# Kernel tuning notes

Measured on AMD Instinct MI355X. Metric: run time of the kernel, lower is better.

Reference implementation:

```python
import jax, jax.numpy as jnp
import numpy as np
import math

D_MODEL = 768
NUM_HEADS = 12
SPARSITY = 0.7


def setup_inputs() -> dict:
    key = jax.random.key(0)
    ks = jax.random.split(key, 9)
    B, S, D = 2, 2048, D_MODEL
    scale = 1.0 / math.sqrt(D)  # xavier-ish
    inp = {
        "x": jax.random.normal(ks[0], (B, S, D), dtype=jnp.float32),
        "Wq": jax.random.normal(ks[1], (D, D), dtype=jnp.float32) * scale,
        "bq": jnp.zeros((D,), dtype=jnp.float32),
        "Wk": jax.random.normal(ks[2], (D, D), dtype=jnp.float32) * scale,
        "bk": jnp.zeros((D,), dtype=jnp.float32),
        "Wv": jax.random.normal(ks[3], (D, D), dtype=jnp.float32) * scale,
        "bv": jnp.zeros((D,), dtype=jnp.float32),
        "Wo": jax.random.normal(ks[4], (D, D), dtype=jnp.float32) * scale,
        "bo": jnp.zeros((D,), dtype=jnp.float32),
    }
    return inp


def reference(x, Wq, bq, Wk, bk, Wv, bv, Wo, bo):
    B, S, D = x.shape
    H = NUM_HEADS
    hd = D // H
    k_keep = max(1, int((1.0 - SPARSITY) * S))

    # projections (nn.Linear: x @ W.T + b), split into heads -> [B,H,S,hd]
    q = (x @ Wq.T + bq).reshape(B, S, H, hd).transpose(0, 2, 1, 3)
    k = (x @ Wk.T + bk).reshape(B, S, H, hd).transpose(0, 2, 1, 3)
    v = (x @ Wv.T + bv).reshape(B, S, H, hd).transpose(0, 2, 1, 3)

    # dense scores [B,H,S,S]
    scores = jnp.einsum("bhqd,bhkd->bhqk", q, k) / math.sqrt(hd)

    # per-row top-k sparsification (training path of the torch module)
    _, topk_idx = jax.lax.top_k(scores, k_keep)  # [B,H,S,k]
    bi = jnp.arange(B)[:, None, None, None]
    hi = jnp.arange(H)[None, :, None, None]
    si = jnp.arange(S)[None, None, :, None]
    keep = jnp.zeros(scores.shape, dtype=bool).at[bi, hi, si, topk_idx].set(True)
    scores = jnp.where(keep, scores, jnp.float32(-1e9))

    attn = jax.nn.softmax(scores, axis=-1)
    out = jnp.einsum("bhqk,bhkd->bhqd", attn, v)  # [B,H,S,hd]
    out = out.transpose(0, 2, 1, 3).reshape(B, S, D)
    return out @ Wo.T + bo
```

## Files before the change

### kernel.cpp

```cpp
#include <hip/hip_runtime.h>
#include <math.h>

#define B_ 2
#define S_ 2048
#define D_ 768
#define H_ 12
#define HD_ 64
#define KKEEP 614
#define M_ (B_*S_)
#define KD_ 768
#define SRW 2072

typedef __attribute__((ext_vector_type(8))) short bf8;
typedef __attribute__((ext_vector_type(4))) float f4;

__device__ __forceinline__ unsigned short f2bf(float f) {
    unsigned u = __float_as_uint(f);
    u += 0x7FFF + ((u >> 16) & 1);
    return (unsigned short)(u >> 16);
}
__device__ __forceinline__ float bf2f(unsigned short h) {
    return __uint_as_float((unsigned)h << 16);
}
__device__ __forceinline__ unsigned pk_sext15(unsigned o) {
    return ((o >> 15) & 0x00010001u) * 0xFFFFu;
}

__global__ void split_kernel(const float* __restrict__ src,
                             unsigned short* __restrict__ hi,
                             unsigned short* __restrict__ lo, int n) {
    int i = blockIdx.x * blockDim.x + threadIdx.x;
    if (i >= n) return;
    float f = src[i];
    unsigned short h = f2bf(f);
    hi[i] = h;
    lo[i] = f2bf(f - bf2f(h));
}

__global__ void split_w_kernel(const float* __restrict__ w0, const float* __restrict__ w1,
                               const float* __restrict__ w2, const float* __restrict__ w3,
                               unsigned short* __restrict__ hi,
                               unsigned short* __restrict__ lo) {
    const int which = blockIdx.y;
    const float* src = which == 0 ? w0 : (which == 1 ? w1 : (which == 2 ? w2 : w3));
    int i = blockIdx.x * blockDim.x + threadIdx.x;
    size_t o = (size_t)which * (D_ * D_) + i;
    float f = src[i];
    unsigned short h = f2bf(f);
    hi[o] = h;
    lo[o] = f2bf(f - bf2f(h));
}

__global__ __launch_bounds__(256)
void gemm_qkv(const unsigned short* __restrict__ Ahi, const unsigned short* __restrict__ Alo,
              const unsigned short* __restrict__ Wch, const unsigned short* __restrict__ Wcl,
              const float* __restrict__ bq, const float* __restrict__ bk,
              const float* __restrict__ bv,
              unsigned short* __restrict__ Qh, unsigned short* __restrict__ Ql,
              unsigned short* __restrict__ Kh, unsigned short* __restrict__ Vth) {
    __shared__ unsigned short Ah[128][32], Al[128][32], Bh[64][32], Bl[64][32];
    const int bm = blockIdx.x * 128, bnG = blockIdx.y * 64;
    const int which = blockIdx.y / 12;
    const int bn = bnG - which * 768;
    const float* bias = which == 0 ? bq : (which == 1 ? bk : bv);
    const int tid = threadIdx.x, lane = tid & 63, wave = tid >> 6;
    const int col = lane & 15, quad = lane >> 4;

    f4 acc[2][4];
#pragma unroll
    for (int mi = 0; mi < 2; ++mi)
#pragma unroll
        for (int ni = 0; ni < 4; ++ni) { f4 z = {0.f,0.f,0.f,0.f}; acc[mi][ni] = z; }

    for (int kt = 0; kt < KD_; kt += 32) {
        __syncthreads();
#pragma unroll
        for (int c = 0; c < 2; ++c) {
            int idx = c * 256 + tid;
            int row = idx >> 2, ko = (idx & 3) * 8;
            *(uint4*)&Ah[row][ko] = *(const uint4*)&Ahi[(size_t)(bm + row) * KD_ + kt + ko];
            *(uint4*)&Al[row][ko] = *(const uint4*)&Alo[(size_t)(bm + row) * KD_ + kt + ko];
        }
        {
            int row = tid >> 2, ko = (tid & 3) * 8;
            *(uint4*)&Bh[row][ko] = *(const uint4*)&Wch[(size_t)(bnG + row) * KD_ + kt + ko];
            *(uint4*)&Bl[row][ko] = *(const uint4*)&Wcl[(size_t)(bnG + row) * KD_ + kt + ko];
        }
        __syncthreads();

        bf8 af[2][2], wf[4][2];
#pragma unroll
        for (int mi = 0; mi < 2; ++mi) {
            int r = wave * 32 + mi * 16 + col;
            af[mi][0] = *(const bf8*)&Ah[r][quad * 8];
            af[mi][1] = *(const bf8*)&Al[r][quad * 8];
        }
#pragma unroll
        for (int ni = 0; ni < 4; ++ni) {
            int r = ni * 16 + col;
            wf[ni][0] = *(const bf8*)&Bh[r][quad * 8];
            wf[ni][1] = *(const bf8*)&Bl[r][quad * 8];
        }
#pragma unroll
        for (int mi = 0; mi < 2; ++mi)
#pragma unroll
            for (int ni = 0; ni < 4; ++ni) {
                acc[mi][ni] = __builtin_amdgcn_mfma_f32_16x16x32_bf16(af[mi][0], wf[ni][0], acc[mi][ni], 0, 0, 0);
                acc[mi][ni] = __builtin_amdgcn_mfma_f32_16x16x32_bf16(af[mi][1], wf[ni][0], acc[mi][ni], 0, 0, 0);
                acc[mi][ni] = __builtin_amdgcn_mfma_f32_16x16x32_bf16(af[mi][0], wf[ni][1], acc[mi][ni], 0, 0, 0);
            }
    }

    float bvv[4];
#pragma unroll
    for (int ni = 0; ni < 4; ++ni) bvv[ni] = bias[bn + ni * 16 + col];
#pragma unroll
    for (int mi = 0; mi < 2; ++mi)
#pragma unroll
        for (int ni = 0; ni < 4; ++ni)
#pragma unroll
            for (int r = 0; r < 4; ++r) {
                int m = bm + wave * 32 + mi * 16 + quad * 4 + r;
                int n = bn + ni * 16 + col;
                float v = acc[mi][ni][r] + bvv[ni];
                if (which == 0) v *= 0.18033688f;
                int b = m >> 11, s = m & 2047, h = n >> 6, d = n & 63;
                unsigned short hh = f2bf(v);
                if (which == 0) {
                    size_t idx = (((size_t)b * H_ + h) * S_ + s) * HD_ + d;
                    Qh[idx] = hh;
                    Ql[idx] = f2bf(v - bf2f(hh));
                } else if (which == 1) {
                    Kh[(((size_t)b * H_ + h) * S_ + s) * HD_ + d] = hh;
                } else {
                    Vth[(((size_t)b * H_ + h) * HD_ + d) * S_ + s] = hh;
                }
            }
}

__global__ __launch_bounds__(256)
void gemm_o(const unsigned short* __restrict__ Ahi, const unsigned short* __restrict__ Alo,
            const unsigned short* __restrict__ Whi, const unsigned short* __restrict__ Wlo,
            const float* __restrict__ bias, float* __restrict__ outf) {
    __shared__ unsigned short Ah[128][32], Al[128][32], Bh[64][32], Bl[64][32];
    const int bm = blockIdx.x * 128, bn = blockIdx.y * 64;
    const int tid = threadIdx.x, lane = tid & 63, wave = tid >> 6;
    const int col = lane & 15, quad = lane >> 4;

    f4 acc[2][4];
#pragma unroll
    for (int mi = 0; mi < 2; ++mi)
#pragma unroll
        for (int ni = 0; ni < 4; ++ni) { f4 z = {0.f,0.f,0.f,0.f}; acc[mi][ni] = z; }

    for (int kt = 0; kt < KD_; kt += 32) {
        __syncthreads();
#pragma unroll
        for (int c = 0; c < 2; ++c) {
            int idx = c * 256 + tid;
            int row = idx >> 2, ko = (idx & 3) * 8;
            *(uint4*)&Ah[row][ko] = *(const uint4*)&Ahi[(size_t)(bm + row) * KD_ + kt + ko];
            *(uint4*)&Al[row][ko] = *(const uint4*)&Alo[(size_t)(bm + row) * KD_ + kt + ko];
        }
        {
            int row = tid >> 2, ko = (tid & 3) * 8;
            *(uint4*)&Bh[row][ko] = *(const uint4*)&Whi[(size_t)(bn + row) * KD_ + kt + ko];
            *(uint4*)&Bl[row][ko] = *(const uint4*)&Wlo[(size_t)(bn + row) * KD_ + kt + ko];
        }
        __syncthreads();

        bf8 af[2][2], wf[4][2];
#pragma unroll
        for (int mi = 0; mi < 2; ++mi) {
            int r = wave * 32 + mi * 16 + col;
            af[mi][0] = *(const bf8*)&Ah[r][quad * 8];
            af[mi][1] = *(const bf8*)&Al[r][quad * 8];
        }
#pragma unroll
        for (int ni = 0; ni < 4; ++ni) {
            int r = ni * 16 + col;
            wf[ni][0] = *(const bf8*)&Bh[r][quad * 8];
            wf[ni][1] = *(const bf8*)&Bl[r][quad * 8];
        }
#pragma unroll
        for (int mi = 0; mi < 2; ++mi)
#pragma unroll
            for (int ni = 0; ni < 4; ++ni) {
                acc[mi][ni] = __builtin_amdgcn_mfma_f32_16x16x32_bf16(af[mi][0], wf[ni][0], acc[mi][ni], 0, 0, 0);
                acc[mi][ni] = __builtin_amdgcn_mfma_f32_16x16x32_bf16(af[mi][1], wf[ni][0], acc[mi][ni], 0, 0, 0);
                acc[mi][ni] = __builtin_amdgcn_mfma_f32_16x16x32_bf16(af[mi][0], wf[ni][1], acc[mi][ni], 0, 0, 0);
            }
    }

    float bvv[4];
#pragma unroll
    for (int ni = 0; ni < 4; ++ni) bvv[ni] = bias[bn + ni * 16 + col];
#pragma unroll
    for (int mi = 0; mi < 2; ++mi)
#pragma unroll
        for (int ni = 0; ni < 4; ++ni)
#pragma unroll
            for (int r = 0; r < 4; ++r) {
                int m = bm + wave * 32 + mi * 16 + quad * 4 + r;
                int n = bn + ni * 16 + col;
                outf[(size_t)m * D_ + n] = acc[mi][ni][r] + bvv[ni];
            }
}

__global__ __launch_bounds__(1024, 8)
void attn_kernel(const unsigned short* __restrict__ Qhi, const unsigned short* __restrict__ Qlo,
                 const unsigned short* __restrict__ Khi,
                 const unsigned short* __restrict__ Vthi,
                 unsigned short* __restrict__ AOhi, unsigned short* __restrict__ AOlo) {
    const int bid = blockIdx.x;
    const int xcd = bid & 7, sub = (bid >> 3) % 3, tile = bid / 24;
    const int bh = xcd * 3 + sub;
    const int b = bh / H_, h = bh % H_;
    const int q0 = tile * 16;
    const int tid = threadIdx.x, lane = tid & 63, wave = tid >> 6;
    const int col = lane & 15, quad = lane >> 4;

    __shared__ __align__(16) unsigned char arena[16 * 4144];
    unsigned short* scB = (unsigned short*)arena;
    float (*osum)[16][64] = (float (*)[16][64])arena;
    __shared__ float linv[16];

    const unsigned short* Qbh = Qhi + (size_t)bh * (S_ * HD_);
    const unsigned short* Qbl = Qlo + (size_t)bh * (S_ * HD_);
    const unsigned qo = (unsigned)((q0 + col) * HD_ + quad * 8);
    bf8 qh0 = *(const bf8*)&Qbh[qo];
    bf8 qh1 = *(const bf8*)&Qbh[qo + 32];
    bf8 ql0 = *(const bf8*)&Qbl[qo];
    bf8 ql1 = *(const bf8*)&Qbl[qo + 32];

    const unsigned short* Kb = Khi + (size_t)bh * (S_ * HD_);
#pragma unroll 4
    for (int t = 0; t < 8; ++t) {
        const unsigned kro = (unsigned)((wave * 128 + t * 16 + col) * HD_ + quad * 8);
        bf8 kh0 = *(const bf8*)&Kb[kro];
        bf8 kh1 = *(const bf8*)&Kb[kro + 32];
        f4 z = {0.f, 0.f, 0.f, 0.f};
        __builtin_amdgcn_s_setprio(1);
        f4 ah = __builtin_amdgcn_mfma_f32_16x16x32_bf16(qh0, kh0, z, 0, 0, 0);
        ah = __builtin_amdgcn_mfma_f32_16x16x32_bf16(qh1, kh1, ah, 0, 0, 0);
        f4 al = __builtin_amdgcn_mfma_f32_16x16x32_bf16(ql0, kh0, z, 0, 0, 0);
        al = __builtin_amdgcn_mfma_f32_16x16x32_bf16(ql1, kh1, al, 0, 0, 0);
        __builtin_amdgcn_s_setprio(0);
        f4 a = ah + al;
        unsigned p01, p23;
        asm("v_cvt_pk_bf16_f32 %0, %1, %2" : "=v"(p01) : "v"(a[0]), "v"(a[1]));
        asm("v_cvt_pk_bf16_f32 %0, %1, %2" : "=v"(p23) : "v"(a[2]), "v"(a[3]));
        unsigned o01 = p01 ^ (pk_sext15(p01) | 0x80008000u);
        unsigned o23 = p23 ^ (pk_sext15(p23) | 0x80008000u);
        const int cp = wave * 128 + t * 16 + col;
        scB[(quad * 4 + 0) * SRW + cp] = (unsigned short)o01;
        scB[(quad * 4 + 1) * SRW + cp] = (unsigned short)(o01 >> 16);
        scB[(quad * 4 + 2) * SRW + cp] = (unsigned short)o23;
        scB[(quad * 4 + 3) * SRW + cp] = (unsigned short)(o23 >> 16);
    }
    __syncthreads();

    unsigned* rowp = (unsigned*)(arena + wave * 4144);
    const unsigned s_swz = ((unsigned)lane >> 1) & 3u;
    unsigned kv[16], kvs[16];
#pragma unroll
    for (int r = 0; r < 4; ++r) {
        uint4 v = *(const uint4*)&rowp[lane * 16 + (((unsigned)r ^ s_swz) << 2)];
        kv[r * 4 + 0] = v.x; kv[r * 4 + 1] = v.y;
        kv[r * 4 + 2] = v.z; kv[r * 4 + 3] = v.w;
    }
#pragma unroll
    for (int j = 0; j < 16; ++j) kvs[j] = kv[j] << 16;

    unsigned Mhi = 0, Mlo = 0;
#pragma unroll
    for (int j = 0; j < 16; ++j) {
        Mhi = kv[j]  > Mhi ? kv[j]  : Mhi;
        Mlo = kvs[j] > Mlo ? kvs[j] : Mlo;
    }
    unsigned mo = (Mhi >> 16) > (Mlo >> 16) ? (Mhi >> 16) : (Mlo >> 16);
#pragma unroll
    for (int off = 1; off < 64; off <<= 1) {
        unsigned v = __shfl_xor((int)mo, off, 64);
        mo = mo > v ? mo : v;
    }

    unsigned lo = 0, hi = mo + 1;
    int cnt_lo = 2048, cnt_hi = 0;
    unsigned T;
    unsigned p1 = (mo > 0x1C0u) ? (mo - 0x1C0u) : 1u;
    unsigned p2 = (mo > 0x100u) ? (mo - 0x100u) : 2u;
    if (p2 <= p1) p2 = p1 + 1;
    while (true) {
        const unsigned c1h = p1 << 16, c2h = p2 << 16;
        int c1 = 0, c2 = 0;
#pragma unroll
        for (int j = 0; j < 16; ++j) {
            c1 += __popcll(__ballot(kv[j]  >= c1h));
            c1 += __popcll(__ballot(kvs[j] >= c1h));
            c2 += __popcll(__ballot(kv[j]  >= c2h));
            c2 += __popcll(__ballot(kvs[j] >= c2h));
        }
        if (c1 == KKEEP) { T = p1; break; }
        if (c2 == KKEEP) { T = p2; break; }
        if (c2 > KKEEP)      { lo = p2; cnt_lo = c2; }
        else if (c1 > KKEEP) { lo = p1; cnt_lo = c1; hi = p2; cnt_hi = c2; }
        else                 { hi = p1; cnt_hi = c1; }
        if (hi - lo <= 1) { T = lo; break; }
        p1 = (lo + hi) >> 1;
        {
            float f = (float)(cnt_lo - KKEEP) / (float)(cnt_lo - cnt_hi);
            unsigned step = (unsigned)((float)(hi - lo) * f);
            p2 = lo + step;
            if (p2 <= lo) p2 = lo + 1;
            if (p2 >= hi) p2 = hi - 1;
        }
        if (p1 > p2) { unsigned tt = p1; p1 = p2; p2 = tt; }
    }
    const unsigned Ts = T << 16;

    const unsigned short* Vb = Vthi + (size_t)bh * (HD_ * S_);
    const unsigned sbw = (unsigned)(wave * 128 + quad * 8);
    bf8 vA0, vA1, vA2, vA3, vB0, vB1, vB2, vB3;
    vA0 = *(const bf8*)&Vb[(unsigned)((0 * 16 + col) * S_) + sbw];
    vA1 = *(const bf8*)&Vb[(unsigned)((1 * 16 + col) * S_) + sbw];
    vA2 = *(const bf8*)&Vb[(unsigned)((2 * 16 + col) * S_) + sbw];
    vA3 = *(const bf8*)&Vb[(unsigned)((3 * 16 + col) * S_) + sbw];

    float ls = 0.f;
#pragma unroll
    for (int g = 0; g < 4; ++g) {
        unsigned wv[4];
#pragma unroll
        for (int u = 0; u < 4; ++u) {
            int j = g * 4 + u;
            unsigned o = kv[j];
            unsigned bits = o ^ (~pk_sext15(o) | 0x80008000u);
            float wl = __uint_as_float(bits << 16);
            float wh = __uint_as_float(bits & 0xFFFF0000u);
            wl = __builtin_amdgcn_exp2f(wl);
            wh = __builtin_amdgcn_exp2f(wh);
            wl = (kvs[j] >= Ts) ? wl : 0.f;
            wh = (o >= Ts) ? wh : 0.f;
            ls += wl + wh;
            unsigned pk;
            asm("v_cvt_pk_bf16_f32 %0, %1, %2" : "=v"(pk) : "v"(wl), "v"(wh));
            wv[u] = pk;
        }
        uint4 ov; ov.x = wv[0]; ov.y = wv[1]; ov.z = wv[2]; ov.w = wv[3];
        *(uint4*)&rowp[lane * 16 + (((unsigned)g ^ s_swz) << 2)] = ov;
    }
#pragma unroll
    for (int off = 1; off < 64; off <<= 1) ls += __shfl_xor(ls, off, 64);
    if (lane == 0) linv[wave] = 1.f / ls;
    __syncthreads();

    f4 od0 = {0.f,0.f,0.f,0.f}, od1 = {0.f,0.f,0.f,0.f};
    f4 od2 = {0.f,0.f,0.f,0.f}, od3 = {0.f,0.f,0.f,0.f};
    const unsigned pvb = (unsigned)(col * SRW + wave * 128 + quad * 8);
    {
        bf8 ph0 = *(const bf8*)&scB[pvb + 0 * 32];
        vB0 = *(const bf8*)&Vb[(unsigned)((0 * 16 + col) * S_) + sbw + 32];
        vB1 = *(const bf8*)&Vb[(unsigned)((1 * 16 + col) * S_) + sbw + 32];
        vB2 = *(const bf8*)&Vb[(unsigned)((2 * 16 + col) * S_) + sbw + 32];
        vB3 = *(const bf8*)&Vb[(unsigned)((3 * 16 + col) * S_) + sbw + 32];
        __builtin_amdgcn_s_setprio(1);
        od0 = __builtin_amdgcn_mfma_f32_16x16x32_bf16(ph0, vA0, od0, 0, 0, 0);
        od1 = __builtin_amdgcn_mfma_f32_16x16x32_bf16(ph0, vA1, od1, 0, 0, 0);
        od2 = __builtin_amdgcn_mfma_f32_16x16x32_bf16(ph0, vA2, od2, 0, 0, 0);
        od3 = __builtin_amdgcn_mfma_f32_16x16x32_bf16(ph0, vA3, od3, 0, 0, 0);
        __builtin_amdgcn_s_setprio(0);

        bf8 ph1 = *(const bf8*)&scB[pvb + 1 * 32];
        vA0 = *(const bf8*)&Vb[(unsigned)((0 * 16 + col) * S_) + sbw + 64];
        vA1 = *(const bf8*)&Vb[(unsigned)((1 * 16 + col) * S_) + sbw + 64];
        vA2 = *(const bf8*)&Vb[(unsigned)((2 * 16 + col) * S_) + sbw + 64];
        vA3 = *(const bf8*)&Vb[(unsigned)((3 * 16 + col) * S_) + sbw + 64];
        __builtin_amdgcn_s_setprio(1);
        od0 = __builtin_amdgcn_mfma_f32_16x16x32_bf16(ph1, vB0, od0, 0, 0, 0);
        od1 = __builtin_amdgcn_mfma_f32_16x16x32_bf16(ph1, vB1, od1, 0, 0, 0);
        od2 = __builtin_amdgcn_mfma_f32_16x16x32_bf16(ph1, vB2, od2, 0, 0, 0);
        od3 = __builtin_amdgcn_mfma_f32_16x16x32_bf16(ph1, vB3, od3, 0, 0, 0);
        __builtin_amdgcn_s_setprio(0);

        bf8 ph2 = *(const bf8*)&scB[pvb + 2 * 32];
        vB0 = *(const bf8*)&Vb[(unsigned)((0 * 16 + col) * S_) + sbw + 96];
        vB1 = *(const bf8*)&Vb[(unsigned)((1 * 16 + col) * S_) + sbw + 96];
        vB2 = *(const bf8*)&Vb[(unsigned)((2 * 16 + col) * S_) + sbw + 96];
        vB3 = *(const bf8*)&Vb[(unsigned)((3 * 16 + col) * S_) + sbw + 96];
        __builtin_amdgcn_s_setprio(1);
        od0 = __builtin_amdgcn_mfma_f32_16x16x32_bf16(ph2, vA0, od0, 0, 0, 0);
        od1 = __builtin_amdgcn_mfma_f32_16x16x32_bf16(ph2, vA1, od1, 0, 0, 0);
        od2 = __builtin_amdgcn_mfma_f32_16x16x32_bf16(ph2, vA2, od2, 0, 0, 0);
        od3 = __builtin_amdgcn_mfma_f32_16x16x32_bf16(ph2, vA3, od3, 0, 0, 0);
        __builtin_amdgcn_s_setprio(0);

        bf8 ph3 = *(const bf8*)&scB[pvb + 3 * 32];
        __builtin_amdgcn_s_setprio(1);
        od0 = __builtin_amdgcn_mfma_f32_16x16x32_bf16(ph3, vB0, od0, 0, 0, 0);
        od1 = __builtin_amdgcn_mfma_f32_16x16x32_bf16(ph3, vB1, od1, 0, 0, 0);
        od2 = __builtin_amdgcn_mfma_f32_16x16x32_bf16(ph3, vB2, od2, 0, 0, 0);
        od3 = __builtin_amdgcn_mfma_f32_16x16x32_bf16(ph3, vB3, od3, 0, 0, 0);
        __builtin_amdgcn_s_setprio(0);
    }
    __syncthreads();
#pragma unroll
    for (int r = 0; r < 4; ++r) {
        osum[wave][quad * 4 + r][0 * 16 + col] = od0[r];
        osum[wave][quad * 4 + r][1 * 16 + col] = od1[r];
        osum[wave][quad * 4 + r][2 * 16 + col] = od2[r];
        osum[wave][quad * 4 + r][3 * 16 + col] = od3[r];
    }
    __syncthreads();

    {
        int q = tid >> 6, d = tid & 63;
        float s = 0.f;
#pragma unroll
        for (int w = 0; w < 16; ++w) s += osum[w][q][d];
        s *= linv[q];
        size_t idx = ((size_t)b * S_ + q0 + q) * D_ + h * HD_ + d;
        unsigned short hh = f2bf(s);
        AOhi[idx] = hh;
        AOlo[idx] = f2bf(s - bf2f(hh));
    }
}

extern "C" void kernel_launch(void* const* d_in, const int* in_sizes, int n_in,
                              void* d_out, int out_size, void* d_ws, size_t ws_size,
                              hipStream_t stream) {
    const float* x  = (const float*)d_in[0];
    const float* Wq = (const float*)d_in[1];
    const float* bq = (const float*)d_in[2];
    const float* Wk = (const float*)d_in[3];
    const float* bk = (const float*)d_in[4];
    const float* Wv = (const float*)d_in[5];
    const float* bv = (const float*)d_in[6];
    const float* Wo = (const float*)d_in[7];
    const float* bo = (const float*)d_in[8];
    float* out = (float*)d_out;

    const size_t NP = (size_t)M_ * D_;
    const size_t NW = (size_t)D_ * D_;
    unsigned short* p = (unsigned short*)d_ws;
    unsigned short* xhi = p;  p += NP;
    unsigned short* xlo = p;  p += NP;
    unsigned short* Wch = p;  p += 4 * NW;
    unsigned short* Wcl = p;  p += 4 * NW;
    unsigned short* Qh  = p;  p += NP;  unsigned short* Ql  = p;  p += NP;
    unsigned short* Kh  = p;  p += NP;
    unsigned short* Vth = p;  p += NP;
    unsigned short* AOh = xhi;
    unsigned short* AOl = xlo;

    split_kernel<<<(int)(NP / 256), 256, 0, stream>>>(x, xhi, xlo, (int)NP);
    {
        dim3 gw((unsigned)(NW / 256), 4);
        split_w_kernel<<<gw, 256, 0, stream>>>(Wq, Wk, Wv, Wo, Wch, Wcl);
    }

    {
        dim3 g(M_ / 128, 36);
        gemm_qkv<<<g, 256, 0, stream>>>(xhi, xlo, Wch, Wcl, bq, bk, bv,
                                        Qh, Ql, Kh, Vth);
    }

    attn_kernel<<<(S_ / 16) * B_ * H_, 1024, 0, stream>>>(Qh, Ql, Kh, Vth, AOh, AOl);

    {
        dim3 g(M_ / 128, D_ / 64);
        gemm_o<<<g, 256, 0, stream>>>(AOh, AOl, Wch + 3 * NW, Wcl + 3 * NW, bo, out);
    }
}
```

Measured before the change: 394.3 us.

## Enlarge QKV GEMM tile to 128x128 and load tiles via direct global-to-LDS

The QKV projection GEMM tile grows from 128x64 to 128x128, with waves arranged 2x2 so each wave computes a 64x64 sub-tile and holds 4x4 accumulators. The grid shrinks from 36 to 18 column blocks. Global-to-shared copies now use the global_load_lds builtin, which skips the register staging. This aims to raise operand reuse per LDS load and cut load instruction overhead, at the cost of more accumulator registers and half as many blocks.

```diff
diff --git a/kernel.cpp b/kernel.cpp
--- a/kernel.cpp
+++ b/kernel.cpp
@@ -24,6 +24,12 @@
 }
 __device__ __forceinline__ unsigned pk_sext15(unsigned o) {
     return ((o >> 15) & 0x00010001u) * 0xFFFFu;
+}
+__device__ __forceinline__ void gload16(const unsigned short* g, unsigned short* l) {
+    __builtin_amdgcn_global_load_lds(
+        (const __attribute__((address_space(1))) unsigned int*)(const void*)g,
+        (__attribute__((address_space(3))) unsigned int*)(void*)l,
+        16, 0, 0);
 }
 
 __global__ void split_kernel(const float* __restrict__ src,
@@ -58,17 +64,18 @@
               const float* __restrict__ bv,
               unsigned short* __restrict__ Qh, unsigned short* __restrict__ Ql,
               unsigned short* __restrict__ Kh, unsigned short* __restrict__ Vth) {
-    __shared__ unsigned short Ah[128][32], Al[128][32], Bh[64][32], Bl[64][32];
-    const int bm = blockIdx.x * 128, bnG = blockIdx.y * 64;
-    const int which = blockIdx.y / 12;
-    const int bn = bnG - which * 768;
+    __shared__ unsigned short Ah[128][32], Al[128][32], Bh[128][32], Bl[128][32];
+    const int bm = blockIdx.x * 128, bnG = blockIdx.y * 128;
+    const int which = blockIdx.y / 6;
+    const int bnl = bnG - which * 768;
     const float* bias = which == 0 ? bq : (which == 1 ? bk : bv);
     const int tid = threadIdx.x, lane = tid & 63, wave = tid >> 6;
     const int col = lane & 15, quad = lane >> 4;
-
-    f4 acc[2][4];
-#pragma unroll
-    for (int mi = 0; mi < 2; ++mi)
+    const int wr = wave >> 1, wc = wave & 1;
+
+    f4 acc[4][4];
+#pragma unroll
+    for (int mi = 0; mi < 4; ++mi)
 #pragma unroll
         for (int ni = 0; ni < 4; ++ni) { f4 z = {0.f,0.f,0.f,0.f}; acc[mi][ni] = z; }
 
@@ -78,31 +85,30 @@
         for (int c = 0; c < 2; ++c) {
             int idx = c * 256 + tid;
             int row = idx >> 2, ko = (idx & 3) * 8;
-            *(uint4*)&Ah[row][ko] = *(const uint4*)&Ahi[(size_t)(bm + row) * KD_ + kt + ko];
-            *(uint4*)&Al[row][ko] = *(const uint4*)&Alo[(size_t)(bm + row) * KD_ + kt + ko];
-        }
-        {
-            int row = tid >> 2, ko = (tid & 3) * 8;
-            *(uint4*)&Bh[row][ko] = *(const uint4*)&Wch[(size_t)(bnG + row) * KD_ + kt + ko];
-            *(uint4*)&Bl[row][ko] = *(const uint4*)&Wcl[(size_t)(bnG + row) * KD_ + kt + ko];
+            size_t ga = (size_t)(bm + row) * KD_ + kt + ko;
+            size_t gb = (size_t)(bnG + row) * KD_ + kt + ko;
+            gload16(&Ahi[ga], &Ah[row][ko]);
+            gload16(&Alo[ga], &Al[row][ko]);
+            gload16(&Wch[gb], &Bh[row][ko]);
+            gload16(&Wcl[gb], &Bl[row][ko]);
         }
         __syncthreads();
 
-        bf8 af[2][2], wf[4][2];
-#pragma unroll
-        for (int mi = 0; mi < 2; ++mi) {
-            int r = wave * 32 + mi * 16 + col;
+        bf8 af[4][2], wf[4][2];
+#pragma unroll
+        for (int mi = 0; mi < 4; ++mi) {
+            int r = wr * 64 + mi * 16 + col;
             af[mi][0] = *(const bf8*)&Ah[r][quad * 8];
             af[mi][1] = *(const bf8*)&Al[r][quad * 8];
         }
 #pragma unroll
         for (int ni = 0; ni < 4; ++ni) {
-            int r = ni * 16 + col;
+            int r = wc * 64 + ni * 16 + col;
             wf[ni][0] = *(const bf8*)&Bh[r][quad * 8];
             wf[ni][1] = *(const bf8*)&Bl[r][quad * 8];
         }
 #pragma unroll
-        for (int mi = 0; mi < 2; ++mi)
+        for (int mi = 0; mi < 4; ++mi)
 #pragma unroll
             for (int ni = 0; ni < 4; ++ni) {
                 acc[mi][ni] = __builtin_amdgcn_mfma_f32_16x16x32_bf16(af[mi][0], wf[ni][0], acc[mi][ni], 0, 0, 0);
@@ -113,15 +119,15 @@
 
     float bvv[4];
 #pragma unroll
-    for (int ni = 0; ni < 4; ++ni) bvv[ni] = bias[bn + ni * 16 + col];
-#pragma unroll
-    for (int mi = 0; mi < 2; ++mi)
+    for (int ni = 0; ni < 4; ++ni) bvv[ni] = bias[bnl + wc * 64 + ni * 16 + col];
+#pragma unroll
+    for (int mi = 0; mi < 4; ++mi)
 #pragma unroll
         for (int ni = 0; ni < 4; ++ni)
 #pragma unroll
             for (int r = 0; r < 4; ++r) {
-                int m = bm + wave * 32 + mi * 16 + quad * 4 + r;
-                int n = bn + ni * 16 + col;
+                int m = bm + wr * 64 + mi * 16 + quad * 4 + r;
+                int n = bnl + wc * 64 + ni * 16 + col;
                 float v = acc[mi][ni][r] + bvv[ni];
                 if (which == 0) v *= 0.18033688f;
                 int b = m >> 11, s = m & 2047, h = n >> 6, d = n & 63;
@@ -460,7 +466,7 @@
     }
 
     {
-        dim3 g(M_ / 128, 36);
+        dim3 g(M_ / 128, 18);
         gemm_qkv<<<g, 256, 0, stream>>>(xhi, xlo, Wch, Wcl, bq, bk, bv,
                                         Qh, Ql, Kh, Vth);
     }
```

New measurement: 403.6 us. 2.4% more time.
